# Kernel tuning notes

Hardware: AMD Instinct MI355X
Metric: run time of the kernel (lower is better)

Reference implementation:

```python
import jax, jax.numpy as jnp
import numpy as np

DIM = 1024
B, L = 4, 4096


def setup_inputs() -> dict:
    key = jax.random.key(0)
    ks = jax.random.split(key, 6)
    s = 1.0 / np.sqrt(DIM)
    x = jax.random.normal(ks[0], (B, L, DIM), dtype=jnp.float32)
    Wk = jax.random.uniform(ks[1], (DIM, DIM), jnp.float32, -s, s)
    bk = jax.random.uniform(ks[2], (DIM,), jnp.float32, -s, s)
    Wv = jax.random.uniform(ks[3], (DIM, DIM), jnp.float32, -s, s)
    bv = jax.random.uniform(ks[4], (DIM,), jnp.float32, -s, s)
    ln_g = jnp.ones((DIM,), jnp.float32)
    ln_b = jnp.zeros((DIM,), jnp.float32)
    Wo = jax.random.uniform(ks[5], (DIM, DIM), jnp.float32, -s, s)
    bo = jnp.zeros((DIM,), jnp.float32)
    return {"x": x, "Wk": Wk, "bk": bk, "Wv": Wv, "bv": bv,
            "ln_g": ln_g, "ln_b": ln_b, "Wo": Wo, "bo": bo}


def reference(x, Wk, bk, Wv, bv, ln_g, ln_b, Wo, bo):
    B_, L_, D = x.shape
    # key/value projections (torch Linear: x @ W.T + b)
    keys = x @ Wk.T + bk
    keys = keys / jnp.maximum(jnp.linalg.norm(keys, axis=-1, keepdims=True), 1e-12)
    values = x @ Wv.T + bv
    # circular convolution via FFT: bind keys with values
    Kf = jnp.fft.rfft(keys, axis=-1)
    Vf = jnp.fft.rfft(values, axis=-1)
    bound = jnp.fft.irfft(Kf * Vf, n=D, axis=-1)
    # cumulative holographic memory over sequence
    memory = jnp.cumsum(bound, axis=1)
    # circular correlation (unbind): conj of key spectrum
    Mf = jnp.fft.rfft(memory, axis=-1)
    retrieved = jnp.fft.irfft(Mf * jnp.conj(Kf), n=D, axis=-1)
    # position-dependent normalization: sqrt(1..L)
    norm = jnp.sqrt(jnp.arange(1, L_ + 1, dtype=x.dtype)).reshape(1, L_, 1)
    r = retrieved / norm
    # LayerNorm (eps=1e-5) + output Linear
    mu = jnp.mean(r, axis=-1, keepdims=True)
    var = jnp.var(r, axis=-1, keepdims=True)
    r_ln = (r - mu) * jax.lax.rsqrt(var + 1e-5) * ln_g + ln_b
    return x + (r_ln @ Wo.T + bo)
```

## Files before the change

kernel.cpp:

```cpp
#include <hip/hip_runtime.h>
#include <math.h>

#define B_SZ 4
#define L_SZ 4096
#define D_SZ 1024
#define M_SZ (B_SZ * L_SZ)
#define NBINS 513
#define CCH   1026
#define PSTR  1028
#define TLEN 8
#define NCH  (L_SZ / TLEN)
#define NG   32

typedef short bf16x8 __attribute__((ext_vector_type(8)));
typedef float f32x4  __attribute__((ext_vector_type(4)));
typedef unsigned short us8 __attribute__((ext_vector_type(8)));

#define AS1 __attribute__((address_space(1)))
#define AS3 __attribute__((address_space(3)))

__device__ inline unsigned short f2bf(float f) {
    unsigned int u = __float_as_uint(f);
    u += 0x7fffu + ((u >> 16) & 1u);
    return (unsigned short)(u >> 16);
}
__device__ inline float bf2f(unsigned short u) {
    return __uint_as_float(((unsigned int)u) << 16);
}

__global__ __launch_bounds__(256) void cast_f32_bf16(
        const float* __restrict__ in, unsigned short* __restrict__ out, int n8) {
    int i = blockIdx.x * 256 + threadIdx.x;
    if (i >= n8) return;
    const float4* p = (const float4*)in + 2 * (size_t)i;
    float4 a = p[0], b = p[1];
    us8 o;
    o[0] = f2bf(a.x); o[1] = f2bf(a.y); o[2] = f2bf(a.z); o[3] = f2bf(a.w);
    o[4] = f2bf(b.x); o[5] = f2bf(b.y); o[6] = f2bf(b.z); o[7] = f2bf(b.w);
    *(us8*)(out + (size_t)i * 8) = o;
}

__global__ __launch_bounds__(256) void cast_w3(
        const float* __restrict__ Wk, const float* __restrict__ Wv,
        const float* __restrict__ Wo,
        unsigned short* __restrict__ WB, unsigned short* __restrict__ Wob, int n8) {
    int i = blockIdx.x * 256 + threadIdx.x;
    if (i >= n8) return;
    const int which = blockIdx.y;
    const float* src = (which == 0) ? Wk : (which == 1) ? Wv : Wo;
    unsigned short* dst = (which == 0) ? WB : (which == 1) ? (WB + D_SZ * D_SZ) : Wob;
    const float4* p = (const float4*)src + 2 * (size_t)i;
    float4 a = p[0], b = p[1];
    us8 o;
    o[0] = f2bf(a.x); o[1] = f2bf(a.y); o[2] = f2bf(a.z); o[3] = f2bf(a.w);
    o[4] = f2bf(b.x); o[5] = f2bf(b.y); o[6] = f2bf(b.z); o[7] = f2bf(b.w);
    *(us8*)(dst + (size_t)i * 8) = o;
}

template<int CNT, bool OBF16>
__global__ __launch_bounds__(512, 4) void gemm_mfma(
        const unsigned short* __restrict__ A, const unsigned short* __restrict__ W,
        const float* __restrict__ bias0, const float* __restrict__ bias1,
        const float* __restrict__ resid,
        void* __restrict__ C0v, void* __restrict__ C1v, int M, int K) {
    __shared__ unsigned short Abuf[3][256 * 32];
    __shared__ unsigned short Bbuf[3][128 * 32];
    const int id   = blockIdx.x;
    const int bx   = (id >> 3) % CNT;
    const int by   = (id & 7) + 8 * (id / (8 * CNT));
    const int tid  = threadIdx.x;
    const int lane = tid & 63;
    const int wid  = tid >> 6;
    const int wr   = wid >> 2;
    const int wc   = wid & 3;
    const int bm   = by * 256;
    const int bn   = bx * 128;

    const int sl = tid >> 3;
    const int sq = (tid & 7) ^ (sl & 7);
    const int srow = 2 * sl + (sq >> 2);
    const int skof = (sq & 3) * 8;
    const unsigned short* Abase = A + (size_t)(bm + srow) * K + skof;
    const unsigned short* Wbase = W + (size_t)(bn + srow) * K + skof;
    const int dstoff = tid * 16;

    auto stage3 = [&](int slot, int kk) {
        __builtin_amdgcn_global_load_lds((const AS1 unsigned int*)(Abase + kk),
            (AS3 unsigned int*)((char*)&Abuf[slot][0] + dstoff), 16, 0, 0);
        __builtin_amdgcn_global_load_lds((const AS1 unsigned int*)(Abase + (size_t)128 * K + kk),
            (AS3 unsigned int*)((char*)&Abuf[slot][128 * 32] + dstoff), 16, 0, 0);
        __builtin_amdgcn_global_load_lds((const AS1 unsigned int*)(Wbase + kk),
            (AS3 unsigned int*)((char*)&Bbuf[slot][0] + dstoff), 16, 0, 0);
    };

    const int fr = lane & 15;
    const int kq = lane >> 4;
    const int rslot = (((((fr & 1) << 2) + kq) ^ ((fr >> 1) & 7)) << 4);
    const int aoff0 = wr * 8192 + (fr >> 1) * 128 + rslot;
    const int boff0 = wc * 2048 + (fr >> 1) * 128 + rslot;

    f32x4 acc[8][2] = {};

    const int nt = K >> 5;
    stage3(0, 0);
    stage3(1, 32);
    asm volatile("s_waitcnt vmcnt(3)" ::: "memory");
    __builtin_amdgcn_s_barrier();
    asm volatile("" ::: "memory");

    int slot = 0, slot2 = 2;
    for (int cur = 0; cur < nt; ++cur) {
        bf16x8 a[8], b[2];
        const char* Ab = (const char*)&Abuf[slot][0];
        const char* Bb = (const char*)&Bbuf[slot][0];
        #pragma unroll
        for (int nf = 0; nf < 2; nf++)
            b[nf] = *(const bf16x8*)(Bb + boff0 + nf * 1024);
        #pragma unroll
        for (int mf = 0; mf < 8; mf++)
            a[mf] = *(const bf16x8*)(Ab + aoff0 + mf * 1024);
        if (cur + 2 < nt) stage3(slot2, (cur + 2) << 5);
        __builtin_amdgcn_s_setprio(1);
        #pragma unroll
        for (int mf = 0; mf < 8; mf++)
            #pragma unroll
            for (int nf = 0; nf < 2; nf++)
                acc[mf][nf] = __builtin_amdgcn_mfma_f32_16x16x32_bf16(
                                  a[mf], b[nf], acc[mf][nf], 0, 0, 0);
        __builtin_amdgcn_s_setprio(0);
        if (cur + 2 < nt) { asm volatile("s_waitcnt vmcnt(3)" ::: "memory"); }
        else              { asm volatile("s_waitcnt vmcnt(0)" ::: "memory"); }
        __builtin_amdgcn_s_barrier();
        asm volatile("" ::: "memory");
        slot  = (slot  == 2) ? 0 : slot  + 1;
        slot2 = (slot2 == 2) ? 0 : slot2 + 1;
    }

    const int col0 = lane & 15;
    const int quad = lane >> 4;
    #pragma unroll
    for (int nf = 0; nf < 2; nf++) {
        const int ng = bn + wc * 32 + nf * 16 + col0;
        const int half = ng >> 10;
        const int n = ng & 1023;
        const float bv = half ? bias1[n] : bias0[n];
        void* Cv = half ? C1v : C0v;
        #pragma unroll
        for (int mf = 0; mf < 8; mf++) {
            #pragma unroll
            for (int r = 0; r < 4; r++) {
                const int m = bm + wr * 128 + mf * 16 + quad * 4 + r;
                float v = acc[mf][nf][r] + bv;
                size_t off = (size_t)m * 1024 + n;
                if constexpr (OBF16) {
                    ((unsigned short*)Cv)[off] = f2bf(v);
                } else {
                    if (resid) v += resid[off];
                    ((float*)Cv)[off] = v;
                }
            }
        }
    }
}

#define SWZ(a) ((a) ^ (((a) >> 4) & 15))

struct cplx { float r, i; };
__device__ inline cplx cmul(cplx a, cplx b) {
    return {a.r * b.r - a.i * b.i, a.r * b.i + a.i * b.r};
}

__device__ inline void r4bfly(cplx v[4], float s) {
    cplx t0 {v[0].r + v[2].r, v[0].i + v[2].i};
    cplx t1 {v[0].r - v[2].r, v[0].i - v[2].i};
    cplx t2 {v[1].r + v[3].r, v[1].i + v[3].i};
    cplx t3 {v[1].r - v[3].r, v[1].i - v[3].i};
    cplx j3 {-s * t3.i, s * t3.r};
    v[0] = {t0.r + t2.r, t0.i + t2.i};
    v[2] = {t0.r - t2.r, t0.i - t2.i};
    v[1] = {t1.r + j3.r, t1.i + j3.i};
    v[3] = {t1.r - j3.r, t1.i - j3.i};
}

template<int SIGN>
__device__ inline void make_w1(cplx w1s[4], int tid) {
    const float s = (float)SIGN;
    #pragma unroll
    for (int q = 1; q <= 3; q++) {
        const int Ls = 1 << (2 * q);
        const float ang = s * 1.57079632679489662f * (float)(tid & (Ls - 1)) / (float)Ls;
        float sn, cs; __sincosf(ang, &sn, &cs);
        w1s[q - 1] = {cs, sn};
    }
    float sn, cs;
    __sincosf(s * 1.57079632679489662f * (float)tid / 256.0f, &sn, &cs);
    w1s[3] = {cs, sn};
}

template<int SIGN>
__device__ inline void fft1024_tw(float2* bA, float2* bB, cplx v[4], int tid,
                                  const cplx w1s[4]) {
    const float s = (float)SIGN;
    r4bfly(v, s);
    {
        const int base = tid << 2;
        #pragma unroll
        for (int e = 0; e < 4; e++)
            bA[SWZ(base + e)] = make_float2(v[e].r, v[e].i);
    }
    __syncthreads();
    float2* cur = bA;
    float2* nxt = bB;
    #pragma unroll
    for (int q = 1; q <= 3; q++) {
        const int Ls = 1 << (2 * q);
        #pragma unroll
        for (int k = 0; k < 4; k++) {
            float2 t = cur[SWZ(tid + (k << 8))];
            v[k] = {t.x, t.y};
        }
        const int d = tid & (Ls - 1);
        cplx w1 = w1s[q - 1];
        cplx w2 = cmul(w1, w1);
        cplx w3 = cmul(w2, w1);
        v[1] = cmul(v[1], w1);
        v[2] = cmul(v[2], w2);
        v[3] = cmul(v[3], w3);
        r4bfly(v, s);
        const int base = ((tid >> (2 * q)) << (2 * q + 2)) + d;
        #pragma unroll
        for (int e = 0; e < 4; e++)
            nxt[SWZ(base + (e << (2 * q)))] = make_float2(v[e].r, v[e].i);
        float2* tmp = cur; cur = nxt; nxt = tmp;
        __syncthreads();
    }
    #pragma unroll
    for (int k = 0; k < 4; k++) {
        float2 t = cur[SWZ(tid + (k << 8))];
        v[k] = {t.x, t.y};
    }
    {
        cplx w1 = w1s[3];
        cplx w2 = cmul(w1, w1);
        cplx w3 = cmul(w2, w1);
        v[1] = cmul(v[1], w1);
        v[2] = cmul(v[2], w2);
        v[3] = cmul(v[3], w3);
        r4bfly(v, s);
    }
}

__global__ __launch_bounds__(256) void bind_cum_kernel(
        unsigned short* __restrict__ KIO, const unsigned short* __restrict__ Vb,
        unsigned short* __restrict__ P, float* __restrict__ totals) {
    __shared__ float2 bA[1024], bB[1024];
    __shared__ unsigned int kvs[1024];
    __shared__ float red[4];
    const int blk = blockIdx.x;
    const int tid = threadIdx.x;
    const int wv  = tid >> 6;
    const int ln  = tid & 63;
    const size_t tok0 = (size_t)blk * TLEN;

    cplx w1s[4];
    make_w1<-1>(w1s, tid);

    float r0r = 0.f, r0i = 0.f, r1r = 0.f, r1i = 0.f, r2r = 0.f, r2i = 0.f;

    ushort4 k4 = *(const ushort4*)(KIO + tok0 * D_SZ + 4 * tid);
    ushort4 v4 = *(const ushort4*)(Vb  + tok0 * D_SZ + 4 * tid);
    {
        uint4 pk;
        pk.x = (unsigned int)k4.x | ((unsigned int)v4.x << 16);
        pk.y = (unsigned int)k4.y | ((unsigned int)v4.y << 16);
        pk.z = (unsigned int)k4.z | ((unsigned int)v4.z << 16);
        pk.w = (unsigned int)k4.w | ((unsigned int)v4.w << 16);
        *(uint4*)&kvs[4 * tid] = pk;
    }
    __syncthreads();

    for (int tk = 0; tk < TLEN; ++tk) {
        const size_t token = tok0 + tk;
        unsigned short* krow = KIO + token * D_SZ;

        float kvC[4], vvC[4];
        float ss = 0.f;
        #pragma unroll
        for (int k = 0; k < 4; k++) {
            unsigned int pk = kvs[tid + (k << 8)];
            kvC[k] = bf2f((unsigned short)(pk & 0xffffu));
            vvC[k] = bf2f((unsigned short)(pk >> 16));
            ss += kvC[k] * kvC[k];
        }
        #pragma unroll
        for (int m = 1; m < 64; m <<= 1) ss += __shfl_xor(ss, m, 64);
        if (ln == 0) red[wv] = ss;
        __syncthreads();
        const float scale = 1.0f /
            fmaxf(sqrtf(red[0] + red[1] + red[2] + red[3]), 1e-12f);

        cplx z[4];
        #pragma unroll
        for (int k = 0; k < 4; k++) z[k] = {kvC[k] * scale, vvC[k]};

        if (tk + 1 < TLEN) {
            k4 = *(const ushort4*)(KIO + (token + 1) * D_SZ + 4 * tid);
            v4 = *(const ushort4*)(Vb  + (token + 1) * D_SZ + 4 * tid);
        }

        fft1024_tw<-1>(bA, bB, z, tid, w1s);

        #pragma unroll
        for (int e = 0; e < 4; e++)
            bA[SWZ(tid + (e << 8))] = make_float2(z[e].r, z[e].i);
        if (tk + 1 < TLEN) {
            uint4 pk;
            pk.x = (unsigned int)k4.x | ((unsigned int)v4.x << 16);
            pk.y = (unsigned int)k4.y | ((unsigned int)v4.y << 16);
            pk.z = (unsigned int)k4.z | ((unsigned int)v4.z << 16);
            pk.w = (unsigned int)k4.w | ((unsigned int)v4.w << 16);
            *(uint4*)&kvs[4 * tid] = pk;
        }
        __syncthreads();

        float ar512 = 0.f;
        if (tid == 0) {
            float2 Zc = bA[SWZ(512)];
            r2r += Zc.x * Zc.y;
            ar512 = Zc.x;
            ushort2 pv; pv.x = f2bf(r2r); pv.y = f2bf(r2i);
            *(ushort2*)(P + token * PSTR + 1024) = pv;
        }

        const int b0 = 2 * tid, b1 = 2 * tid + 1;
        float ar0, ai0, ar1, ai1;
        {
            float2 Zb = bA[SWZ(b0)];
            float2 Zm = bA[SWZ((1024 - b0) & 1023)];
            ar0 = 0.5f * (Zb.x + Zm.x);
            ai0 = 0.5f * (Zb.y - Zm.y);
            float br = 0.5f * (Zb.y + Zm.y);
            float bi = 0.5f * (Zm.x - Zb.x);
            r0r += ar0 * br - ai0 * bi;
            r0i += ar0 * bi + ai0 * br;
        }
        {
            float2 Zb = bA[SWZ(b1)];
            float2 Zm = bA[SWZ(1024 - b1)];
            ar1 = 0.5f * (Zb.x + Zm.x);
            ai1 = 0.5f * (Zb.y - Zm.y);
            float br = 0.5f * (Zb.y + Zm.y);
            float bi = 0.5f * (Zm.x - Zb.x);
            r1r += ar1 * br - ai1 * bi;
            r1i += ar1 * bi + ai1 * br;
        }
        ushort4 pw;
        pw.x = f2bf(r0r); pw.y = f2bf(r0i);
        pw.z = f2bf(r1r); pw.w = f2bf(r1i);
        *(ushort4*)(P + token * PSTR + 4 * tid) = pw;
        ushort4 kfw;
        kfw.x = f2bf(ar0);
        kfw.y = (tid == 0) ? f2bf(ar512) : f2bf(ai0);
        kfw.z = f2bf(ar1); kfw.w = f2bf(ai1);
        *(ushort4*)(krow + 4 * tid) = kfw;
    }

    float* trow = totals + (size_t)blk * PSTR;
    float4 tw; tw.x = r0r; tw.y = r0i; tw.z = r1r; tw.w = r1i;
    *(float4*)(trow + 4 * tid) = tw;
    if (tid == 0) { trow[1024] = r2r; trow[1025] = r2i; }
}

__global__ __launch_bounds__(256) void scan_s1(
        float* __restrict__ totals, float* __restrict__ gt) {
    const int c = blockIdx.x * 256 + threadIdx.x;
    if (c >= CCH) return;
    const int g = blockIdx.y;
    const int b = blockIdx.z;
    float run = 0.f;
    #pragma unroll
    for (int i = 0; i < 16; i++) {
        size_t idx = ((size_t)(b * NCH + g * 16 + i)) * PSTR + c;
        float v = totals[idx];
        totals[idx] = run;
        run += v;
    }
    gt[((size_t)(b * NG + g)) * PSTR + c] = run;
}

__global__ __launch_bounds__(256) void scan_s2(float* __restrict__ gt) {
    const int c = blockIdx.x * 256 + threadIdx.x;
    if (c >= CCH) return;
    const int b = blockIdx.y;
    float run = 0.f;
    #pragma unroll
    for (int g = 0; g < NG; g++) {
        size_t idx = ((size_t)(b * NG + g)) * PSTR + c;
        float v = gt[idx];
        gt[idx] = run;
        run += v;
    }
}

__global__ __launch_bounds__(256) void unbind4_ln_kernel(
        const unsigned short* __restrict__ P, const float* __restrict__ totals,
        const float* __restrict__ gt, const unsigned short* __restrict__ KF,
        const float* __restrict__ ln_g, const float* __restrict__ ln_b,
        unsigned short* __restrict__ RLNb) {
    __shared__ float2 bA[1024], bB[1024];
    __shared__ __align__(16) float2 offsh[514];
    __shared__ float red[16];
    const int blk = blockIdx.x;
    const int tid = threadIdx.x;
    const int wv  = tid >> 6;
    const int ln  = tid & 63;
    const size_t tok0 = (size_t)blk * TLEN;
    const int bidx  = (int)(tok0 >> 12);
    const int t0    = (int)(tok0 & (L_SZ - 1));
    const int chunk = t0 >> 3;

    {
        const float* off2 = totals + (size_t)(bidx * NCH + chunk) * PSTR;
        const float* gof2 = gt + (size_t)(bidx * NG + (chunk >> 4)) * PSTR;
        float4 o = *(const float4*)(off2 + 4 * tid);
        float4 g = *(const float4*)(gof2 + 4 * tid);
        float4 og; og.x = o.x + g.x; og.y = o.y + g.y;
        og.z = o.z + g.z; og.w = o.w + g.w;
        *(float4*)&offsh[2 * tid] = og;
        if (tid == 0)
            offsh[512] = make_float2(off2[1024] + gof2[1024],
                                     off2[1025] + gof2[1025]);
    }

    cplx w1s[4];
    make_w1<1>(w1s, tid);

    float gv[4], bev[4];
    #pragma unroll
    for (int e = 0; e < 4; e++) {
        gv[e]  = ln_g[tid + (e << 8)];
        bev[e] = ln_b[tid + (e << 8)];
    }
    __syncthreads();

    const int b0 = 2 * tid, b1 = 2 * tid + 1;

    for (int p = 0; p < 4; ++p) {
        const size_t ta = tok0 + 2 * p, tb = ta + 1;
        const unsigned short* Pa = P + ta * PSTR;
        const unsigned short* Pc = P + tb * PSTR;
        const unsigned short* Ka = KF + ta * D_SZ;
        const unsigned short* Kc = KF + tb * D_SZ;

        ushort4 sa = *(const ushort4*)(Pa + 4 * tid);
        ushort4 sb = *(const ushort4*)(Pc + 4 * tid);
        ushort4 ka = *(const ushort4*)(Ka + 4 * tid);
        ushort4 kb = *(const ushort4*)(Kc + 4 * tid);
        float2 og0 = offsh[b0], og1 = offsh[b1];

        {
            float ka_r = bf2f(ka.x), ka_i = (tid == 0) ? 0.f : bf2f(ka.y);
            float kb_r = bf2f(kb.x), kb_i = (tid == 0) ? 0.f : bf2f(kb.y);
            float sra = bf2f(sa.x) + og0.x, sia = bf2f(sa.y) + og0.y;
            float srb = bf2f(sb.x) + og0.x, sib = bf2f(sb.y) + og0.y;
            float Zar = sra * ka_r + sia * ka_i, Zai = sia * ka_r - sra * ka_i;
            float Zbr = srb * kb_r + sib * kb_i, Zbi = sib * kb_r - srb * kb_i;
            bA[SWZ(b0)] = make_float2(Zar - Zbi, Zai + Zbr);
            if (b0 != 0)
                bA[SWZ(1024 - b0)] = make_float2(Zar + Zbi, Zbr - Zai);
        }
        {
            float ka_r = bf2f(ka.z), ka_i = bf2f(ka.w);
            float kb_r = bf2f(kb.z), kb_i = bf2f(kb.w);
            float sra = bf2f(sa.z) + og1.x, sia = bf2f(sa.w) + og1.y;
            float srb = bf2f(sb.z) + og1.x, sib = bf2f(sb.w) + og1.y;
            float Zar = sra * ka_r + sia * ka_i, Zai = sia * ka_r - sra * ka_i;
            float Zbr = srb * kb_r + sib * kb_i, Zbi = sib * kb_r - srb * kb_i;
            bA[SWZ(b1)] = make_float2(Zar - Zbi, Zai + Zbr);
            bA[SWZ(1024 - b1)] = make_float2(Zar + Zbi, Zbr - Zai);
        }
        if (tid == 0) {
            ushort2 s5a = *(const ushort2*)(Pa + 1024);
            ushort2 s5b = *(const ushort2*)(Pc + 1024);
            float2 og = offsh[512];
            float kra = bf2f(Ka[1]), krb = bf2f(Kc[1]);
            float sra = bf2f(s5a.x) + og.x, sia = bf2f(s5a.y) + og.y;
            float srb = bf2f(s5b.x) + og.x, sib = bf2f(s5b.y) + og.y;
            float Zar = sra * kra, Zai = sia * kra;
            float Zbr = srb * krb, Zbi = sib * krb;
            bA[SWZ(512)] = make_float2(Zar - Zbi, Zai + Zbr);
        }
        __syncthreads();

        cplx z[4];
        #pragma unroll
        for (int k = 0; k < 4; k++) {
            float2 c = bA[SWZ(tid + (k << 8))];
            z[k] = {c.x, c.y};
        }
        __syncthreads();
        fft1024_tw<1>(bA, bB, z, tid, w1s);

        const int t_a = t0 + 2 * p;
        const float sc_a = (1.0f / 1024.0f) * rsqrtf((float)(t_a + 1));
        const float sc_b = (1.0f / 1024.0f) * rsqrtf((float)(t_a + 2));
        float ra[4], rb[4];
        float s1a = 0.f, s2a = 0.f, s1b = 0.f, s2b = 0.f;
        #pragma unroll
        for (int e = 0; e < 4; e++) {
            ra[e] = z[e].r * sc_a;
            rb[e] = z[e].i * sc_b;
            s1a += ra[e]; s2a += ra[e] * ra[e];
            s1b += rb[e]; s2b += rb[e] * rb[e];
        }
        #pragma unroll
        for (int m = 1; m < 64; m <<= 1) {
            s1a += __shfl_xor(s1a, m, 64);
            s2a += __shfl_xor(s2a, m, 64);
            s1b += __shfl_xor(s1b, m, 64);
            s2b += __shfl_xor(s2b, m, 64);
        }
        if (ln == 0) {
            red[wv] = s1a; red[4 + wv] = s2a; red[8 + wv] = s1b; red[12 + wv] = s2b;
        }
        __syncthreads();
        const float S1a = red[0] + red[1] + red[2] + red[3];
        const float S2a = red[4] + red[5] + red[6] + red[7];
        const float S1b = red[8] + red[9] + red[10] + red[11];
        const float S2b = red[12] + red[13] + red[14] + red[15];
        const float mua = S1a * (1.0f / 1024.0f);
        const float vara = S2a * (1.0f / 1024.0f) - mua * mua;
        const float rsa = rsqrtf(vara + 1e-5f);
        const float mub = S1b * (1.0f / 1024.0f);
        const float varb = S2b * (1.0f / 1024.0f) - mub * mub;
        const float rsb = rsqrtf(varb + 1e-5f);

        unsigned short* outA = RLNb + ta * D_SZ;
        unsigned short* outB = RLNb + tb * D_SZ;
        #pragma unroll
        for (int e = 0; e < 4; e++) {
            const int d = tid + (e << 8);
            outA[d] = f2bf((ra[e] - mua) * rsa * gv[e] + bev[e]);
            outB[d] = f2bf((rb[e] - mub) * rsb * gv[e] + bev[e]);
        }
        __syncthreads();
    }
}

extern "C" void kernel_launch(void* const* d_in, const int* in_sizes, int n_in,
                              void* d_out, int out_size, void* d_ws, size_t ws_size,
                              hipStream_t stream) {
    (void)in_sizes; (void)n_in; (void)out_size; (void)ws_size;
    const float* x    = (const float*)d_in[0];
    const float* Wk   = (const float*)d_in[1];
    const float* bk   = (const float*)d_in[2];
    const float* Wv   = (const float*)d_in[3];
    const float* bv   = (const float*)d_in[4];
    const float* ln_g = (const float*)d_in[5];
    const float* ln_b = (const float*)d_in[6];
    const float* Wo   = (const float*)d_in[7];
    const float* bo   = (const float*)d_in[8];
    float* out = (float*)d_out;

    char* w = (char*)d_ws;
    unsigned short* Kb  = (unsigned short*)w;  w += (size_t)M_SZ * D_SZ * 2;
    unsigned short* Vb  = (unsigned short*)w;  w += (size_t)M_SZ * D_SZ * 2;
    unsigned short* Pb  = (unsigned short*)w;  w += (size_t)M_SZ * PSTR * 2;
    unsigned short* xb  = (unsigned short*)w;  w += (size_t)M_SZ * D_SZ * 2;
    unsigned short* WB  = (unsigned short*)w;  w += (size_t)2 * D_SZ * D_SZ * 2;
    unsigned short* Wob = (unsigned short*)w;  w += (size_t)D_SZ * D_SZ * 2;
    unsigned short* RLNb = Vb;
    float* totals = (float*)xb;
    float* gt     = (float*)xb + (size_t)B_SZ * NCH * PSTR;

    const int n8x = M_SZ * D_SZ / 8;
    const int n8w = D_SZ * D_SZ / 8;
    cast_f32_bf16<<<n8x / 256, 256, 0, stream>>>(x, xb, n8x);
    dim3 wgrid(n8w / 256, 3);
    cast_w3<<<wgrid, 256, 0, stream>>>(Wk, Wv, Wo, WB, Wob, n8w);

    gemm_mfma<16, true><<<(M_SZ / 256) * 16, 512, 0, stream>>>(
        xb, WB, bk, bv, nullptr, Kb, Vb, M_SZ, D_SZ);

    bind_cum_kernel<<<M_SZ / TLEN, 256, 0, stream>>>(Kb, Vb, Pb, totals);

    dim3 g1((CCH + 255) / 256, NG, B_SZ);
    scan_s1<<<g1, 256, 0, stream>>>(totals, gt);
    dim3 g2((CCH + 255) / 256, B_SZ);
    scan_s2<<<g2, 256, 0, stream>>>(gt);

    unbind4_ln_kernel<<<M_SZ / TLEN, 256, 0, stream>>>(
        Pb, totals, gt, Kb, ln_g, ln_b, RLNb);

    gemm_mfma<8, false><<<(M_SZ / 256) * 8, 512, 0, stream>>>(
        RLNb, Wob, bo, bo, x, out, out, M_SZ, D_SZ);
}
```

Baseline: 379.0 us.

## Merge cast kernels, retile GEMM warps, double-buffer reductions to drop barriers

Merges the input and weight fp32-to-bf16 casts into a single launch. Changes the GEMM warp layout from 2x4 warps with 128x32 tiles each to 4x2 warps with 64x64 tiles each, so each warp loads fewer LDS fragments per MFMA. In the bind and unbind kernels, reduction scratch is double-buffered and the FFT staging buffer is switched so that some __syncthreads barriers can be removed, with key normalisation folded into the later spectrum math. Removing barriers risks LDS races if the buffer reuse reasoning is wrong.

Measured after the change: 362.0 us. 1.05x faster.

```diff
diff --git a/kernel.cpp b/kernel.cpp
--- a/kernel.cpp
+++ b/kernel.cpp
@@ -28,33 +28,34 @@
     return __uint_as_float(((unsigned int)u) << 16);
 }
 
-__global__ __launch_bounds__(256) void cast_f32_bf16(
-        const float* __restrict__ in, unsigned short* __restrict__ out, int n8) {
-    int i = blockIdx.x * 256 + threadIdx.x;
-    if (i >= n8) return;
-    const float4* p = (const float4*)in + 2 * (size_t)i;
-    float4 a = p[0], b = p[1];
+#define XBLK 8192
+#define WBLK 512
+__global__ __launch_bounds__(256) void cast_all(
+        const float* __restrict__ x, const float* __restrict__ Wk,
+        const float* __restrict__ Wv, const float* __restrict__ Wo,
+        unsigned short* __restrict__ xb, unsigned short* __restrict__ WB,
+        unsigned short* __restrict__ Wob) {
+    const int b = blockIdx.x;
+    const float* src;
+    unsigned short* dst;
+    size_t i;
+    if (b < XBLK) {
+        src = x;  dst = xb;  i = (size_t)b * 256 + threadIdx.x;
+    } else if (b < XBLK + WBLK) {
+        src = Wk; dst = WB;  i = (size_t)(b - XBLK) * 256 + threadIdx.x;
+    } else if (b < XBLK + 2 * WBLK) {
+        src = Wv; dst = WB + D_SZ * D_SZ;
+        i = (size_t)(b - XBLK - WBLK) * 256 + threadIdx.x;
+    } else {
+        src = Wo; dst = Wob;
+        i = (size_t)(b - XBLK - 2 * WBLK) * 256 + threadIdx.x;
+    }
+    const float4* p = (const float4*)src + 2 * i;
+    float4 a = p[0], bb = p[1];
     us8 o;
-    o[0] = f2bf(a.x); o[1] = f2bf(a.y); o[2] = f2bf(a.z); o[3] = f2bf(a.w);
-    o[4] = f2bf(b.x); o[5] = f2bf(b.y); o[6] = f2bf(b.z); o[7] = f2bf(b.w);
-    *(us8*)(out + (size_t)i * 8) = o;
-}
-
-__global__ __launch_bounds__(256) void cast_w3(
-        const float* __restrict__ Wk, const float* __restrict__ Wv,
-        const float* __restrict__ Wo,
-        unsigned short* __restrict__ WB, unsigned short* __restrict__ Wob, int n8) {
-    int i = blockIdx.x * 256 + threadIdx.x;
-    if (i >= n8) return;
-    const int which = blockIdx.y;
-    const float* src = (which == 0) ? Wk : (which == 1) ? Wv : Wo;
-    unsigned short* dst = (which == 0) ? WB : (which == 1) ? (WB + D_SZ * D_SZ) : Wob;
-    const float4* p = (const float4*)src + 2 * (size_t)i;
-    float4 a = p[0], b = p[1];
-    us8 o;
-    o[0] = f2bf(a.x); o[1] = f2bf(a.y); o[2] = f2bf(a.z); o[3] = f2bf(a.w);
-    o[4] = f2bf(b.x); o[5] = f2bf(b.y); o[6] = f2bf(b.z); o[7] = f2bf(b.w);
-    *(us8*)(dst + (size_t)i * 8) = o;
+    o[0] = f2bf(a.x);  o[1] = f2bf(a.y);  o[2] = f2bf(a.z);  o[3] = f2bf(a.w);
+    o[4] = f2bf(bb.x); o[5] = f2bf(bb.y); o[6] = f2bf(bb.z); o[7] = f2bf(bb.w);
+    *(us8*)(dst + i * 8) = o;
 }
 
 template<int CNT, bool OBF16>
@@ -71,8 +72,8 @@
     const int tid  = threadIdx.x;
     const int lane = tid & 63;
     const int wid  = tid >> 6;
-    const int wr   = wid >> 2;
-    const int wc   = wid & 3;
+    const int wr   = wid >> 1;
+    const int wc   = wid & 1;
     const int bm   = by * 256;
     const int bn   = bx * 128;
 
@@ -96,10 +97,10 @@
     const int fr = lane & 15;
     const int kq = lane >> 4;
     const int rslot = (((((fr & 1) << 2) + kq) ^ ((fr >> 1) & 7)) << 4);
-    const int aoff0 = wr * 8192 + (fr >> 1) * 128 + rslot;
-    const int boff0 = wc * 2048 + (fr >> 1) * 128 + rslot;
-
-    f32x4 acc[8][2] = {};
+    const int aoff0 = wr * 4096 + (fr >> 1) * 128 + rslot;
+    const int boff0 = wc * 4096 + (fr >> 1) * 128 + rslot;
+
+    f32x4 acc[4][4] = {};
 
     const int nt = K >> 5;
     stage3(0, 0);
@@ -110,21 +111,21 @@
 
     int slot = 0, slot2 = 2;
     for (int cur = 0; cur < nt; ++cur) {
-        bf16x8 a[8], b[2];
+        bf16x8 a[4], b[4];
         const char* Ab = (const char*)&Abuf[slot][0];
         const char* Bb = (const char*)&Bbuf[slot][0];
         #pragma unroll
-        for (int nf = 0; nf < 2; nf++)
+        for (int nf = 0; nf < 4; nf++)
             b[nf] = *(const bf16x8*)(Bb + boff0 + nf * 1024);
         #pragma unroll
-        for (int mf = 0; mf < 8; mf++)
+        for (int mf = 0; mf < 4; mf++)
             a[mf] = *(const bf16x8*)(Ab + aoff0 + mf * 1024);
         if (cur + 2 < nt) stage3(slot2, (cur + 2) << 5);
         __builtin_amdgcn_s_setprio(1);
         #pragma unroll
-        for (int mf = 0; mf < 8; mf++)
+        for (int mf = 0; mf < 4; mf++)
             #pragma unroll
-            for (int nf = 0; nf < 2; nf++)
+            for (int nf = 0; nf < 4; nf++)
                 acc[mf][nf] = __builtin_amdgcn_mfma_f32_16x16x32_bf16(
                                   a[mf], b[nf], acc[mf][nf], 0, 0, 0);
         __builtin_amdgcn_s_setprio(0);
@@ -139,17 +140,17 @@
     const int col0 = lane & 15;
     const int quad = lane >> 4;
     #pragma unroll
-    for (int nf = 0; nf < 2; nf++) {
-        const int ng = bn + wc * 32 + nf * 16 + col0;
+    for (int nf = 0; nf < 4; nf++) {
+        const int ng = bn + wc * 64 + nf * 16 + col0;
         const int half = ng >> 10;
         const int n = ng & 1023;
         const float bv = half ? bias1[n] : bias0[n];
         void* Cv = half ? C1v : C0v;
         #pragma unroll
-        for (int mf = 0; mf < 8; mf++) {
+        for (int mf = 0; mf < 4; mf++) {
             #pragma unroll
             for (int r = 0; r < 4; r++) {
-                const int m = bm + wr * 128 + mf * 16 + quad * 4 + r;
+                const int m = bm + wr * 64 + mf * 16 + quad * 4 + r;
                 float v = acc[mf][nf][r] + bv;
                 size_t off = (size_t)m * 1024 + n;
                 if constexpr (OBF16) {
@@ -255,7 +256,7 @@
         unsigned short* __restrict__ P, float* __restrict__ totals) {
     __shared__ float2 bA[1024], bB[1024];
     __shared__ unsigned int kvs[1024];
-    __shared__ float red[4];
+    __shared__ float red[2][4];
     const int blk = blockIdx.x;
     const int tid = threadIdx.x;
     const int wv  = tid >> 6;
@@ -294,14 +295,11 @@
         }
         #pragma unroll
         for (int m = 1; m < 64; m <<= 1) ss += __shfl_xor(ss, m, 64);
-        if (ln == 0) red[wv] = ss;
-        __syncthreads();
-        const float scale = 1.0f /
-            fmaxf(sqrtf(red[0] + red[1] + red[2] + red[3]), 1e-12f);
+        if (ln == 0) red[tk & 1][wv] = ss;
 
         cplx z[4];
         #pragma unroll
-        for (int k = 0; k < 4; k++) z[k] = {kvC[k] * scale, vvC[k]};
+        for (int k = 0; k < 4; k++) z[k] = {kvC[k], vvC[k]};
 
         if (tk + 1 < TLEN) {
             k4 = *(const ushort4*)(KIO + (token + 1) * D_SZ + 4 * tid);
@@ -312,7 +310,7 @@
 
         #pragma unroll
         for (int e = 0; e < 4; e++)
-            bA[SWZ(tid + (e << 8))] = make_float2(z[e].r, z[e].i);
+            bB[SWZ(tid + (e << 8))] = make_float2(z[e].r, z[e].i);
         if (tk + 1 < TLEN) {
             uint4 pk;
             pk.x = (unsigned int)k4.x | ((unsigned int)v4.x << 16);
@@ -323,11 +321,16 @@
         }
         __syncthreads();
 
+        const float* rd = red[tk & 1];
+        const float scale = 1.0f /
+            fmaxf(sqrtf(rd[0] + rd[1] + rd[2] + rd[3]), 1e-12f);
+
         float ar512 = 0.f;
         if (tid == 0) {
-            float2 Zc = bA[SWZ(512)];
-            r2r += Zc.x * Zc.y;
-            ar512 = Zc.x;
+            float2 Zc = bB[SWZ(512)];
+            float ark = scale * Zc.x;
+            r2r += ark * Zc.y;
+            ar512 = ark;
             ushort2 pv; pv.x = f2bf(r2r); pv.y = f2bf(r2i);
             *(ushort2*)(P + token * PSTR + 1024) = pv;
         }
@@ -335,20 +338,20 @@
         const int b0 = 2 * tid, b1 = 2 * tid + 1;
         float ar0, ai0, ar1, ai1;
         {
-            float2 Zb = bA[SWZ(b0)];
-            float2 Zm = bA[SWZ((1024 - b0) & 1023)];
-            ar0 = 0.5f * (Zb.x + Zm.x);
-            ai0 = 0.5f * (Zb.y - Zm.y);
+            float2 Zb = bB[SWZ(b0)];
+            float2 Zm = bB[SWZ((1024 - b0) & 1023)];
+            ar0 = scale * 0.5f * (Zb.x + Zm.x);
+            ai0 = scale * 0.5f * (Zb.y - Zm.y);
             float br = 0.5f * (Zb.y + Zm.y);
             float bi = 0.5f * (Zm.x - Zb.x);
             r0r += ar0 * br - ai0 * bi;
             r0i += ar0 * bi + ai0 * br;
         }
         {
-            float2 Zb = bA[SWZ(b1)];
-            float2 Zm = bA[SWZ(1024 - b1)];
-            ar1 = 0.5f * (Zb.x + Zm.x);
-            ai1 = 0.5f * (Zb.y - Zm.y);
+            float2 Zb = bB[SWZ(b1)];
+            float2 Zm = bB[SWZ(1024 - b1)];
+            ar1 = scale * 0.5f * (Zb.x + Zm.x);
+            ai1 = scale * 0.5f * (Zb.y - Zm.y);
             float br = 0.5f * (Zb.y + Zm.y);
             float bi = 0.5f * (Zm.x - Zb.x);
             r1r += ar1 * br - ai1 * bi;
@@ -409,7 +412,7 @@
         unsigned short* __restrict__ RLNb) {
     __shared__ float2 bA[1024], bB[1024];
     __shared__ __align__(16) float2 offsh[514];
-    __shared__ float red[16];
+    __shared__ float red[2][16];
     const int blk = blockIdx.x;
     const int tid = threadIdx.x;
     const int wv  = tid >> 6;
@@ -465,9 +468,9 @@
             float srb = bf2f(sb.x) + og0.x, sib = bf2f(sb.y) + og0.y;
             float Zar = sra * ka_r + sia * ka_i, Zai = sia * ka_r - sra * ka_i;
             float Zbr = srb * kb_r + sib * kb_i, Zbi = sib * kb_r - srb * kb_i;
-            bA[SWZ(b0)] = make_float2(Zar - Zbi, Zai + Zbr);
+            bB[SWZ(b0)] = make_float2(Zar - Zbi, Zai + Zbr);
             if (b0 != 0)
-                bA[SWZ(1024 - b0)] = make_float2(Zar + Zbi, Zbr - Zai);
+                bB[SWZ(1024 - b0)] = make_float2(Zar + Zbi, Zbr - Zai);
         }
         {
             float ka_r = bf2f(ka.z), ka_i = bf2f(ka.w);
@@ -476,8 +479,8 @@
             float srb = bf2f(sb.z) + og1.x, sib = bf2f(sb.w) + og1.y;
             float Zar = sra * ka_r + sia * ka_i, Zai = sia * ka_r - sra * ka_i;
             float Zbr = srb * kb_r + sib * kb_i, Zbi = sib * kb_r - srb * kb_i;
-            bA[SWZ(b1)] = make_float2(Zar - Zbi, Zai + Zbr);
-            bA[SWZ(1024 - b1)] = make_float2(Zar + Zbi, Zbr - Zai);
+            bB[SWZ(b1)] = make_float2(Zar - Zbi, Zai + Zbr);
+            bB[SWZ(1024 - b1)] = make_float2(Zar + Zbi, Zbr - Zai);
         }
         if (tid == 0) {
             ushort2 s5a = *(const ushort2*)(Pa + 1024);
@@ -488,17 +491,16 @@
             float srb = bf2f(s5b.x) + og.x, sib = bf2f(s5b.y) + og.y;
             float Zar = sra * kra, Zai = sia * kra;
             float Zbr = srb * krb, Zbi = sib * krb;
-            bA[SWZ(512)] = make_float2(Zar - Zbi, Zai + Zbr);
+            bB[SWZ(512)] = make_float2(Zar - Zbi, Zai + Zbr);
         }
         __syncthreads();
 
         cplx z[4];
         #pragma unroll
         for (int k = 0; k < 4; k++) {
-            float2 c = bA[SWZ(tid + (k << 8))];
+            float2 c = bB[SWZ(tid + (k << 8))];
             z[k] = {c.x, c.y};
         }
-        __syncthreads();
         fft1024_tw<1>(bA, bB, z, tid, w1s);
 
         const int t_a = t0 + 2 * p;
@@ -520,14 +522,15 @@
             s1b += __shfl_xor(s1b, m, 64);
             s2b += __shfl_xor(s2b, m, 64);
         }
+        float* rw = red[p & 1];
         if (ln == 0) {
-            red[wv] = s1a; red[4 + wv] = s2a; red[8 + wv] = s1b; red[12 + wv] = s2b;
+            rw[wv] = s1a; rw[4 + wv] = s2a; rw[8 + wv] = s1b; rw[12 + wv] = s2b;
         }
         __syncthreads();
-        const float S1a = red[0] + red[1] + red[2] + red[3];
-        const float S2a = red[4] + red[5] + red[6] + red[7];
-        const float S1b = red[8] + red[9] + red[10] + red[11];
-        const float S2b = red[12] + red[13] + red[14] + red[15];
+        const float S1a = rw[0] + rw[1] + rw[2] + rw[3];
+        const float S2a = rw[4] + rw[5] + rw[6] + rw[7];
+        const float S1b = rw[8] + rw[9] + rw[10] + rw[11];
+        const float S2b = rw[12] + rw[13] + rw[14] + rw[15];
         const float mua = S1a * (1.0f / 1024.0f);
         const float vara = S2a * (1.0f / 1024.0f) - mua * mua;
         const float rsa = rsqrtf(vara + 1e-5f);
@@ -543,7 +546,6 @@
             outA[d] = f2bf((ra[e] - mua) * rsa * gv[e] + bev[e]);
             outB[d] = f2bf((rb[e] - mub) * rsb * gv[e] + bev[e]);
         }
-        __syncthreads();
     }
 }
 
@@ -573,11 +575,7 @@
     float* totals = (float*)xb;
     float* gt     = (float*)xb + (size_t)B_SZ * NCH * PSTR;
 
-    const int n8x = M_SZ * D_SZ / 8;
-    const int n8w = D_SZ * D_SZ / 8;
-    cast_f32_bf16<<<n8x / 256, 256, 0, stream>>>(x, xb, n8x);
-    dim3 wgrid(n8w / 256, 3);
-    cast_w3<<<wgrid, 256, 0, stream>>>(Wk, Wv, Wo, WB, Wob, n8w);
+    cast_all<<<XBLK + 3 * WBLK, 256, 0, stream>>>(x, Wk, Wv, Wo, xb, WB, Wob);
 
     gemm_mfma<16, true><<<(M_SZ / 256) * 16, 512, 0, stream>>>(
         xb, WB, bk, bv, nullptr, Kb, Vb, M_SZ, D_SZ);
```
